# Optimization experiments

Measured on AMD Instinct MI355X. Metric: run time of the kernel, lower is better.

The kernel has to match this reference:

```python
import jax, jax.numpy as jnp
import numpy as np

B, S, D, H = 2, 2048, 1024, 16
HD = D // H


def setup_inputs() -> dict:
    key = jax.random.key(0)
    ks = jax.random.split(key, 9)
    s = 1.0 / np.sqrt(D)
    inp = {
        "x": jax.random.normal(ks[0], (B, S, D), dtype=jnp.float32),
        "Wq": jax.random.uniform(ks[1], (D, D), jnp.float32, -s, s),
        "bq": jax.random.uniform(ks[2], (D,), jnp.float32, -s, s),
        "Wk": jax.random.uniform(ks[3], (D, D), jnp.float32, -s, s),
        "bk": jax.random.uniform(ks[4], (D,), jnp.float32, -s, s),
        "Wv": jax.random.uniform(ks[5], (D, D), jnp.float32, -s, s),
        "bv": jax.random.uniform(ks[6], (D,), jnp.float32, -s, s),
        "Wo": jax.random.uniform(ks[7], (D, D), jnp.float32, -s, s),
        "bo": jax.random.uniform(ks[8], (D,), jnp.float32, -s, s),
    }
    return inp


def reference(x, Wq, bq, Wk, bk, Wv, bv, Wo, bo):
    # Linear projections (torch Linear: y = x @ W.T + b)
    q = x @ Wq.T + bq  # [B,S,D]
    k = x @ Wk.T + bk
    v = x @ Wv.T + bv
    # split heads -> [B,H,S,HD]
    q = q.reshape(B, S, H, HD).transpose(0, 2, 1, 3)
    k = k.reshape(B, S, H, HD).transpose(0, 2, 1, 3)
    v = v.reshape(B, S, H, HD).transpose(0, 2, 1, 3)
    scores = jnp.einsum('bhqd,bhkd->bhqk', q, k) / jnp.sqrt(jnp.float32(HD))
    attn = jax.nn.softmax(scores, axis=-1)
    o = jnp.einsum('bhqk,bhkd->bhqd', attn, v)  # [B,H,S,HD]
    o = o.transpose(0, 2, 1, 3).reshape(B, S, D)
    return o @ Wo.T + bo
```

## Files before the change

kernel.cpp:

```cpp
#include <hip/hip_runtime.h>
#include <hip/hip_bf16.h>
#include <stdint.h>


typedef __attribute__((ext_vector_type(8))) short bf16x8;
typedef __attribute__((ext_vector_type(4))) float f32x4;
typedef __attribute__((ext_vector_type(4))) float floatx4;
typedef __attribute__((ext_vector_type(4))) short shortx4;

#define MFMA16(a, b, c) __builtin_amdgcn_mfma_f32_16x16x32_bf16((a), (b), (c), 0, 0, 0)

static __device__ __forceinline__ short f2bf(float f) {
  __hip_bfloat16 h = __float2bfloat16(f);
  return *reinterpret_cast<short*>(&h);
}

static __device__ __forceinline__ float fexp2(float x) {
#if __has_builtin(__builtin_amdgcn_exp2f)
  return __builtin_amdgcn_exp2f(x);
#else
  return exp2f(x);
#endif
}

static __device__ __forceinline__ void gload_lds16(const void* g, void* l) {
  __builtin_amdgcn_global_load_lds(
      (__attribute__((address_space(1))) void*)(void*)g,
      (__attribute__((address_space(3))) void*)l, 16, 0, 0);
}

__global__ void convert_kernel(const float* __restrict__ x,
                               const float* __restrict__ Wq, const float* __restrict__ Wk,
                               const float* __restrict__ Wv, const float* __restrict__ Wo,
                               const float* __restrict__ bq, const float* __restrict__ bk,
                               const float* __restrict__ bv,
                               __hip_bfloat16* __restrict__ xb,
                               __hip_bfloat16* __restrict__ wqkv,
                               __hip_bfloat16* __restrict__ wob,
                               float* __restrict__ bcat) {
  const int NX = (4096 * 1024) / 4;
  const int NW = (1024 * 1024) / 4;
  const int total = NX + 4 * NW;
  for (long i = (long)blockIdx.x * blockDim.x + threadIdx.x; i < total + 768;
       i += (long)gridDim.x * blockDim.x) {
    if (i < total) {
      const float* src;
      __hip_bfloat16* dst;
      long off;
      if (i < NX)             { src = x;  dst = xb;                       off = i; }
      else if (i < NX + NW)   { src = Wq; dst = wqkv;                     off = i - NX; }
      else if (i < NX + 2*NW) { src = Wk; dst = wqkv + 1024 * 1024;       off = i - NX - NW; }
      else if (i < NX + 3*NW) { src = Wv; dst = wqkv + 2 * 1024 * 1024;   off = i - NX - 2*NW; }
      else                    { src = Wo; dst = wob;                      off = i - NX - 3*NW; }
      floatx4 v = *(const floatx4*)(src + off * 4);
      shortx4 sv;
      sv.x = f2bf(v.x); sv.y = f2bf(v.y); sv.z = f2bf(v.z); sv.w = f2bf(v.w);
      *(shortx4*)(dst + off * 4) = sv;
    } else {
      int j = (int)(i - total);
#pragma unroll
      for (int u = 0; u < 4; ++u) {
        int n = j * 4 + u;
        float b = (n < 1024) ? bq[n] : (n < 2048 ? bk[n - 1024] : bv[n - 2048]);
        bcat[n] = b;
      }
    }
  }
}

template <bool OUT_BF16>
__global__ __launch_bounds__(256, 2) void gemm_bt(const __hip_bfloat16* __restrict__ A,
                                                  const __hip_bfloat16* __restrict__ Bm,
                                                  const float* __restrict__ bias,
                                                  void* __restrict__ Cout, int M, int N, int K,
                                                  float scale, int scale_limit) {
  __shared__ __hip_bfloat16 As[128 * 64];
  __shared__ __hip_bfloat16 Bs[128 * 64];
  const int tid = threadIdx.x;
  const int lane = tid & 63;
  const int w = tid >> 6;
  const int wm = w >> 1, wn = w & 1;

  const int nwg = gridDim.x;
  const int bi = blockIdx.x;
  const int wg = (bi & 7) * (nwg >> 3) + (bi >> 3);
  const int MT = M >> 7;
  const int tm = wg % MT, tn = wg / MT;
  const long brow = (long)tm * 128, bcol = (long)tn * 128;

  const int srow = tid >> 3;
  const int scsw = (tid & 7) << 4;

  f32x4 acc[4][4] = {};

  char* lAs = (char*)As + (tid & 0xC0) * 16;
  char* lBs = (char*)Bs + (tid & 0xC0) * 16;

  for (int k0 = 0; k0 < K; k0 += 64) {
#pragma unroll
    for (int p = 0; p < 4; ++p) {
      int r = p * 32 + srow;
      int cb = scsw ^ ((r & 7) << 4);
      gload_lds16(A + (brow + r) * (long)K + k0 + (cb >> 1), lAs + p * 4096);
      gload_lds16(Bm + (bcol + r) * (long)K + k0 + (cb >> 1), lBs + p * 4096);
    }
    __syncthreads();
#pragma unroll
    for (int ks = 0; ks < 2; ++ks) {
      bf16x8 af[4], bfr[4];
      const int cbase = ks * 64 + ((lane >> 4) << 4);
#pragma unroll
      for (int m = 0; m < 4; ++m) {
        int r = wm * 64 + m * 16 + (lane & 15);
        af[m] = *(const bf16x8*)((const char*)As + r * 128 + (cbase ^ ((r & 7) << 4)));
      }
#pragma unroll
      for (int n = 0; n < 4; ++n) {
        int r = wn * 64 + n * 16 + (lane & 15);
        bfr[n] = *(const bf16x8*)((const char*)Bs + r * 128 + (cbase ^ ((r & 7) << 4)));
      }
#pragma unroll
      for (int m = 0; m < 4; ++m)
#pragma unroll
        for (int n = 0; n < 4; ++n) acc[m][n] = MFMA16(af[m], bfr[n], acc[m][n]);
    }
    __syncthreads();
  }

#pragma unroll
  for (int n = 0; n < 4; ++n) {
    const long col = bcol + wn * 64 + n * 16 + (lane & 15);
    const float bv = bias[col];
    const float sc = (col < scale_limit) ? scale : 1.0f;
#pragma unroll
    for (int m = 0; m < 4; ++m) {
      const long row0 = brow + wm * 64 + m * 16 + ((lane >> 4) << 2);
#pragma unroll
      for (int j = 0; j < 4; ++j) {
        float v = (acc[m][n][j] + bv) * sc;
        if (OUT_BF16)
          ((__hip_bfloat16*)Cout)[(row0 + j) * N + col] = __float2bfloat16(v);
        else
          ((float*)Cout)[(row0 + j) * N + col] = v;
      }
    }
  }
}

__global__ __launch_bounds__(256, 2) void attn_kernel(const __hip_bfloat16* __restrict__ qkv,
                                                      __hip_bfloat16* __restrict__ O) {
  __shared__ __hip_bfloat16 Ks[128 * 64];
  __shared__ __hip_bfloat16 Vt[64 * 128];
  __shared__ __hip_bfloat16 Pl[128 * 128];

  const int tid = threadIdx.x;
  const int lane = tid & 63;
  const int w = tid >> 6;
  const int bi = blockIdx.x;
  const int qt = bi & 15, hh = (bi >> 4) & 15, bb = bi >> 8;
  const long rowQ0 = (long)bb * 2048 + qt * 128;
  const long rowK0 = (long)bb * 2048;
  const int qcol = hh * 64, kcol = 1024 + hh * 64, vcol = 2048 + hh * 64;

  bf16x8 qf[2][2];
#pragma unroll
  for (int m = 0; m < 2; ++m)
#pragma unroll
    for (int ks = 0; ks < 2; ++ks) {
      long r = rowQ0 + w * 32 + m * 16 + (lane & 15);
      int c = qcol + ks * 32 + ((lane >> 4) << 3);
      qf[m][ks] = *(const bf16x8*)(qkv + r * 3072 + c);
    }

  f32x4 acc_o[2][4] = {};
  float mrun[8], lrun[8];
#pragma unroll
  for (int i = 0; i < 8; ++i) { mrun[i] = -1e30f; lrun[i] = 0.f; }

  const int srow = tid >> 3;
  const int scsw = (tid & 7) << 4;
  char* lKs = (char*)Ks + (tid & 0xC0) * 16;
  const int vr = tid >> 1;
  const int vc0 = (tid & 1) * 32;

  for (int t = 0; t < 16; ++t) {
    const long kv0 = (long)t * 128;
#pragma unroll
    for (int p = 0; p < 4; ++p) {
      int r = p * 32 + srow;
      int cb = scsw ^ ((r & 7) << 4);
      gload_lds16(qkv + (rowK0 + kv0 + r) * 3072 + kcol + (cb >> 1), lKs + p * 4096);
    }
#pragma unroll
    for (int u = 0; u < 4; ++u) {
      bf16x8 v = *(const bf16x8*)(qkv + (rowK0 + kv0 + vr) * 3072 + vcol + vc0 + u * 8);
#pragma unroll
      for (int e = 0; e < 8; ++e) {
        int d = vc0 + u * 8 + e;
        int blk = (vr >> 3) ^ (d & 15);
        *(short*)((char*)Vt + d * 256 + blk * 16 + ((vr & 7) << 1)) = v[e];
      }
    }
    __syncthreads();

    f32x4 s[2][8] = {};
#pragma unroll
    for (int ks = 0; ks < 2; ++ks) {
      bf16x8 kf[8];
      const int cbase = ks * 64 + ((lane >> 4) << 4);
#pragma unroll
      for (int n = 0; n < 8; ++n) {
        int r = n * 16 + (lane & 15);
        kf[n] = *(const bf16x8*)((const char*)Ks + r * 128 + (cbase ^ ((r & 7) << 4)));
      }
#pragma unroll
      for (int m = 0; m < 2; ++m)
#pragma unroll
        for (int n = 0; n < 8; ++n) s[m][n] = MFMA16(qf[m][ks], kf[n], s[m][n]);
    }

    float corr[2][4];
#pragma unroll
    for (int m = 0; m < 2; ++m)
#pragma unroll
      for (int j = 0; j < 4; ++j) {
        const int idx = m * 4 + j;
        float mx = s[m][0][j];
#pragma unroll
        for (int n = 1; n < 8; ++n) mx = fmaxf(mx, s[m][n][j]);
        mx = fmaxf(mx, __shfl_xor(mx, 1));
        mx = fmaxf(mx, __shfl_xor(mx, 2));
        mx = fmaxf(mx, __shfl_xor(mx, 4));
        mx = fmaxf(mx, __shfl_xor(mx, 8));
        float newm = fmaxf(mrun[idx], mx);
        float c = fexp2(mrun[idx] - newm);
        corr[m][j] = c;
        mrun[idx] = newm;
        float rs = 0.f;
#pragma unroll
        for (int n = 0; n < 8; ++n) {
          float p = fexp2(s[m][n][j] - newm);
          s[m][n][j] = p;
          rs += p;
        }
        rs += __shfl_xor(rs, 1);
        rs += __shfl_xor(rs, 2);
        rs += __shfl_xor(rs, 4);
        rs += __shfl_xor(rs, 8);
        lrun[idx] = lrun[idx] * c + rs;
      }
#pragma unroll
    for (int m = 0; m < 2; ++m)
#pragma unroll
      for (int n = 0; n < 4; ++n)
#pragma unroll
        for (int j = 0; j < 4; ++j) acc_o[m][n][j] *= corr[m][j];

#pragma unroll
    for (int m = 0; m < 2; ++m)
#pragma unroll
      for (int n = 0; n < 8; ++n)
#pragma unroll
        for (int j = 0; j < 4; ++j) {
          int rp = w * 32 + m * 16 + ((lane >> 4) << 2) + j;
          int cbyte = n * 32 + ((lane & 15) << 1);
          int blk = (cbyte >> 4) ^ (rp & 15);
          *(short*)((char*)Pl + rp * 256 + blk * 16 + (cbyte & 15)) = f2bf(s[m][n][j]);
        }
    __syncthreads();

#pragma unroll
    for (int ks = 0; ks < 4; ++ks) {
      bf16x8 pf[2], vf[4];
#pragma unroll
      for (int m = 0; m < 2; ++m) {
        int rp = w * 32 + m * 16 + (lane & 15);
        int blk = (ks * 4 + (lane >> 4)) ^ (rp & 15);
        pf[m] = *(const bf16x8*)((const char*)Pl + rp * 256 + blk * 16);
      }
#pragma unroll
      for (int n = 0; n < 4; ++n) {
        int d = n * 16 + (lane & 15);
        int blk = (ks * 4 + (lane >> 4)) ^ (d & 15);
        vf[n] = *(const bf16x8*)((const char*)Vt + d * 256 + blk * 16);
      }
#pragma unroll
      for (int m = 0; m < 2; ++m)
#pragma unroll
        for (int n = 0; n < 4; ++n) acc_o[m][n] = MFMA16(pf[m], vf[n], acc_o[m][n]);
    }
    __syncthreads();
  }

#pragma unroll
  for (int m = 0; m < 2; ++m)
#pragma unroll
    for (int j = 0; j < 4; ++j) {
      const int idx = m * 4 + j;
      const float inv = 1.0f / lrun[idx];
      const long r = rowQ0 + w * 32 + m * 16 + ((lane >> 4) << 2) + j;
#pragma unroll
      for (int n = 0; n < 4; ++n) {
        int d = n * 16 + (lane & 15);
        O[r * 1024 + qcol + d] = __float2bfloat16(acc_o[m][n][j] * inv);
      }
    }
}

extern "C" void kernel_launch(void* const* d_in, const int* in_sizes, int n_in,
                              void* d_out, int out_size, void* d_ws, size_t ws_size,
                              hipStream_t stream) {
  const float* x  = (const float*)d_in[0];
  const float* Wq = (const float*)d_in[1];
  const float* bq = (const float*)d_in[2];
  const float* Wk = (const float*)d_in[3];
  const float* bk = (const float*)d_in[4];
  const float* Wv = (const float*)d_in[5];
  const float* bv = (const float*)d_in[6];
  const float* Wo = (const float*)d_in[7];
  const float* bo = (const float*)d_in[8];

  __hip_bfloat16* ws = (__hip_bfloat16*)d_ws;
  __hip_bfloat16* xb   = ws;
  __hip_bfloat16* wqkv = xb + (size_t)4096 * 1024;
  __hip_bfloat16* wob  = wqkv + (size_t)3072 * 1024;
  __hip_bfloat16* qkvb = wob + (size_t)1024 * 1024;
  __hip_bfloat16* ob   = qkvb + (size_t)4096 * 3072;
  float* bcat = (float*)(ob + (size_t)4096 * 1024);

  const float qscale = 0.18033688011112042f;

  convert_kernel<<<dim3(2048), dim3(256), 0, stream>>>(x, Wq, Wk, Wv, Wo, bq, bk, bv,
                                                       xb, wqkv, wob, bcat);
  gemm_bt<true><<<dim3(768), dim3(256), 0, stream>>>(xb, wqkv, bcat, (void*)qkvb,
                                                     4096, 3072, 1024, qscale, 1024);
  attn_kernel<<<dim3(512), dim3(256), 0, stream>>>(qkvb, ob);
  gemm_bt<false><<<dim3(256), dim3(256), 0, stream>>>(ob, wob, bo, d_out,
                                                      4096, 1024, 1024, 1.0f, 0);
}
```

Measured before the change: 237.5 us.

## Keep softmax probabilities in registers by computing transposed scores, dropping P LDS

```diff
diff --git a/kernel.cpp b/kernel.cpp
--- a/kernel.cpp
+++ b/kernel.cpp
@@ -13,6 +13,10 @@
 static __device__ __forceinline__ short f2bf(float f) {
   __hip_bfloat16 h = __float2bfloat16(f);
   return *reinterpret_cast<short*>(&h);
+}
+
+static __device__ __forceinline__ uint32_t pack_bf16(float a, float b) {
+  return (uint32_t)(uint16_t)f2bf(a) | ((uint32_t)(uint16_t)f2bf(b) << 16);
 }
 
 static __device__ __forceinline__ float fexp2(float x) {
@@ -151,11 +155,12 @@
                                                       __hip_bfloat16* __restrict__ O) {
   __shared__ __hip_bfloat16 Ks[128 * 64];
   __shared__ __hip_bfloat16 Vt[64 * 128];
-  __shared__ __hip_bfloat16 Pl[128 * 128];
 
   const int tid = threadIdx.x;
   const int lane = tid & 63;
   const int w = tid >> 6;
+  const int g = lane >> 4;
+  const int t = lane & 15;
   const int bi = blockIdx.x;
   const int qt = bi & 15, hh = (bi >> 4) & 15, bb = bi >> 8;
   const long rowQ0 = (long)bb * 2048 + qt * 128;
@@ -167,24 +172,27 @@
   for (int m = 0; m < 2; ++m)
 #pragma unroll
     for (int ks = 0; ks < 2; ++ks) {
-      long r = rowQ0 + w * 32 + m * 16 + (lane & 15);
-      int c = qcol + ks * 32 + ((lane >> 4) << 3);
+      long r = rowQ0 + w * 32 + m * 16 + t;
+      int c = qcol + ks * 32 + g * 8;
       qf[m][ks] = *(const bf16x8*)(qkv + r * 3072 + c);
     }
 
   f32x4 acc_o[2][4] = {};
-  float mrun[8], lrun[8];
-#pragma unroll
-  for (int i = 0; i < 8; ++i) { mrun[i] = -1e30f; lrun[i] = 0.f; }
+  float mrun[2] = {-1e30f, -1e30f}, lrun[2] = {0.f, 0.f};
+  uint32_t cpk[2][8][2];
+
+  const int sb = (lane & 48) | ((lane & 48) >> 2);
 
   const int srow = tid >> 3;
   const int scsw = (tid & 7) << 4;
   char* lKs = (char*)Ks + (tid & 0xC0) * 16;
   const int vr = tid >> 1;
   const int vc0 = (tid & 1) * 32;
-
-  for (int t = 0; t < 16; ++t) {
-    const long kv0 = (long)t * 128;
+  const int vphib = 4 * (vr >> 5) + ((vr >> 2) & 3);
+  const int vinb = ((vr >> 4) & 1) * 8 + (vr & 3) * 2;
+
+  for (int tt = 0; tt < 16; ++tt) {
+    const long kv0 = (long)tt * 128;
 #pragma unroll
     for (int p = 0; p < 4; ++p) {
       int r = p * 32 + srow;
@@ -197,114 +205,94 @@
 #pragma unroll
       for (int e = 0; e < 8; ++e) {
         int d = vc0 + u * 8 + e;
-        int blk = (vr >> 3) ^ (d & 15);
-        *(short*)((char*)Vt + d * 256 + blk * 16 + ((vr & 7) << 1)) = v[e];
+        *(short*)((char*)Vt + d * 256 + ((vphib ^ (d & 15)) << 4) + vinb) = v[e];
       }
     }
     __syncthreads();
 
-    f32x4 s[2][8] = {};
-#pragma unroll
-    for (int ks = 0; ks < 2; ++ks) {
-      bf16x8 kf[8];
-      const int cbase = ks * 64 + ((lane >> 4) << 4);
-#pragma unroll
-      for (int n = 0; n < 8; ++n) {
-        int r = n * 16 + (lane & 15);
-        kf[n] = *(const bf16x8*)((const char*)Ks + r * 128 + (cbase ^ ((r & 7) << 4)));
-      }
-#pragma unroll
-      for (int m = 0; m < 2; ++m)
-#pragma unroll
-        for (int n = 0; n < 8; ++n) s[m][n] = MFMA16(qf[m][ks], kf[n], s[m][n]);
-    }
-
-    float corr[2][4];
-#pragma unroll
-    for (int m = 0; m < 2; ++m)
-#pragma unroll
-      for (int j = 0; j < 4; ++j) {
-        const int idx = m * 4 + j;
-        float mx = s[m][0][j];
-#pragma unroll
-        for (int n = 1; n < 8; ++n) mx = fmaxf(mx, s[m][n][j]);
-        mx = fmaxf(mx, __shfl_xor(mx, 1));
-        mx = fmaxf(mx, __shfl_xor(mx, 2));
-        mx = fmaxf(mx, __shfl_xor(mx, 4));
-        mx = fmaxf(mx, __shfl_xor(mx, 8));
-        float newm = fmaxf(mrun[idx], mx);
-        float c = fexp2(mrun[idx] - newm);
-        corr[m][j] = c;
-        mrun[idx] = newm;
-        float rs = 0.f;
+#pragma unroll
+    for (int m = 0; m < 2; ++m) {
+      f32x4 s[8] = {};
+#pragma unroll
+      for (int ks = 0; ks < 2; ++ks) {
+        const int cbase = ks * 64 + g * 16;
 #pragma unroll
         for (int n = 0; n < 8; ++n) {
-          float p = fexp2(s[m][n][j] - newm);
-          s[m][n][j] = p;
+          int r = n * 16 + t;
+          bf16x8 kf = *(const bf16x8*)((const char*)Ks + r * 128 + (cbase ^ ((r & 7) << 4)));
+          s[n] = MFMA16(kf, qf[m][ks], s[n]);
+        }
+      }
+      float mx = s[0][0];
+#pragma unroll
+      for (int n = 0; n < 8; ++n)
+#pragma unroll
+        for (int j = 0; j < 4; ++j) mx = fmaxf(mx, s[n][j]);
+      mx = fmaxf(mx, __shfl_xor(mx, 16));
+      mx = fmaxf(mx, __shfl_xor(mx, 32));
+      const float newm = fmaxf(mrun[m], mx);
+      const float corr = fexp2(mrun[m] - newm);
+      mrun[m] = newm;
+      float rs = 0.f;
+#pragma unroll
+      for (int n = 0; n < 8; ++n)
+#pragma unroll
+        for (int j = 0; j < 4; ++j) {
+          float p = fexp2(s[n][j] - newm);
+          s[n][j] = p;
           rs += p;
         }
-        rs += __shfl_xor(rs, 1);
-        rs += __shfl_xor(rs, 2);
-        rs += __shfl_xor(rs, 4);
-        rs += __shfl_xor(rs, 8);
-        lrun[idx] = lrun[idx] * c + rs;
-      }
-#pragma unroll
-    for (int m = 0; m < 2; ++m)
-#pragma unroll
-      for (int n = 0; n < 4; ++n)
-#pragma unroll
-        for (int j = 0; j < 4; ++j) acc_o[m][n][j] *= corr[m][j];
-
-#pragma unroll
-    for (int m = 0; m < 2; ++m)
-#pragma unroll
-      for (int n = 0; n < 8; ++n)
-#pragma unroll
-        for (int j = 0; j < 4; ++j) {
-          int rp = w * 32 + m * 16 + ((lane >> 4) << 2) + j;
-          int cbyte = n * 32 + ((lane & 15) << 1);
-          int blk = (cbyte >> 4) ^ (rp & 15);
-          *(short*)((char*)Pl + rp * 256 + blk * 16 + (cbyte & 15)) = f2bf(s[m][n][j]);
-        }
+      rs += __shfl_xor(rs, 16);
+      rs += __shfl_xor(rs, 32);
+      lrun[m] = lrun[m] * corr + rs;
+#pragma unroll
+      for (int j = 0; j < 4; ++j) {
+        float cj = __shfl(corr, sb | j);
+#pragma unroll
+        for (int nd = 0; nd < 4; ++nd) acc_o[m][nd][j] *= cj;
+      }
+#pragma unroll
+      for (int n = 0; n < 8; ++n) {
+        cpk[m][n][0] = pack_bf16(s[n][0], s[n][1]);
+        cpk[m][n][1] = pack_bf16(s[n][2], s[n][3]);
+      }
+    }
+
+#pragma unroll
+    for (int ks = 0; ks < 4; ++ks) {
+      bf16x8 vf[4];
+#pragma unroll
+      for (int nd = 0; nd < 4; ++nd) {
+        int d = nd * 16 + t;
+        vf[nd] = *(const bf16x8*)((const char*)Vt + d * 256 + (((4 * ks + g) ^ t) << 4));
+      }
+#pragma unroll
+      for (int m = 0; m < 2; ++m) {
+        union { bf16x8 v; uint32_t u[4]; } au;
+        au.u[0] = cpk[m][2 * ks][0];
+        au.u[1] = cpk[m][2 * ks][1];
+        au.u[2] = cpk[m][2 * ks + 1][0];
+        au.u[3] = cpk[m][2 * ks + 1][1];
+#pragma unroll
+        for (int nd = 0; nd < 4; ++nd) acc_o[m][nd] = MFMA16(au.v, vf[nd], acc_o[m][nd]);
+      }
+    }
     __syncthreads();
-
-#pragma unroll
-    for (int ks = 0; ks < 4; ++ks) {
-      bf16x8 pf[2], vf[4];
-#pragma unroll
-      for (int m = 0; m < 2; ++m) {
-        int rp = w * 32 + m * 16 + (lane & 15);
-        int blk = (ks * 4 + (lane >> 4)) ^ (rp & 15);
-        pf[m] = *(const bf16x8*)((const char*)Pl + rp * 256 + blk * 16);
-      }
-#pragma unroll
-      for (int n = 0; n < 4; ++n) {
-        int d = n * 16 + (lane & 15);
-        int blk = (ks * 4 + (lane >> 4)) ^ (d & 15);
-        vf[n] = *(const bf16x8*)((const char*)Vt + d * 256 + blk * 16);
-      }
-#pragma unroll
-      for (int m = 0; m < 2; ++m)
-#pragma unroll
-        for (int n = 0; n < 4; ++n) acc_o[m][n] = MFMA16(pf[m], vf[n], acc_o[m][n]);
-    }
-    __syncthreads();
-  }
-
-#pragma unroll
-  for (int m = 0; m < 2; ++m)
+  }
+
+#pragma unroll
+  for (int m = 0; m < 2; ++m) {
+    const float inv = 1.0f / lrun[m];
 #pragma unroll
     for (int j = 0; j < 4; ++j) {
-      const int idx = m * 4 + j;
-      const float inv = 1.0f / lrun[idx];
-      const long r = rowQ0 + w * 32 + m * 16 + ((lane >> 4) << 2) + j;
-#pragma unroll
-      for (int n = 0; n < 4; ++n) {
-        int d = n * 16 + (lane & 15);
-        O[r * 1024 + qcol + d] = __float2bfloat16(acc_o[m][n][j] * inv);
-      }
-    }
+      const float ij = __shfl(inv, sb | j);
+      const long r = rowQ0 + w * 32 + m * 16 + g * 4 + j;
+#pragma unroll
+      for (int nd = 0; nd < 4; ++nd) {
+        O[r * 1024 + qcol + nd * 16 + t] = __float2bfloat16(acc_o[m][nd][j] * ij);
+      }
+    }
+  }
 }
 
 extern "C" void kernel_launch(void* const* d_in, const int* in_sizes, int n_in,
```

New measurement: 198.6 us. -16.4%, faster.
